# Kernel tuning notes

Hardware: AMD Instinct MI355X
Metric: run time of the kernel (lower is better)

Reference implementation:

```python
import jax, jax.numpy as jnp
import numpy as np

FRAME_T = 8
NUM_K = 10


def _masked_att(att, temp):
    # att: [B, H, P, P] -> softmax over groups of size P//FRAME_T, top-k threshold mask
    B, H, P, _ = att.shape
    D = P // FRAME_T
    a = att.reshape(B, H, P, FRAME_T, D)
    a = jax.nn.softmax(a / temp, axis=-1)
    # k-th largest value per row as threshold (torch.topk values are sorted desc)
    margin = jax.lax.top_k(a, NUM_K)[0][..., -1]  # [B,H,P,FRAME_T]
    a = a * (a >= margin[..., None])
    return a  # [B,H,P,FRAME_T,D]


def setup_inputs() -> dict:
    key = jax.random.key(0)
    k1, k2, k3, k4 = jax.random.split(key, 4)
    B, H, P, hd = 4, 12, 1568, 64
    return {
        "att_s": jax.random.normal(k1, (B, H, P, P), dtype=jnp.float32),
        "att_t": jax.random.normal(k2, (B, H, P, P), dtype=jnp.float32),
        "v_s": jax.random.normal(k3, (B, H, P, hd), dtype=jnp.float32),
        "v_t": jax.random.normal(k4, (B, H, P, hd), dtype=jnp.float32),
    }


def reference(att_s, att_t, v_s, v_t):
    temp = jnp.float32(1.0)
    B, H, P, _ = att_t.shape
    H_s = att_s.shape[1]
    h_dim = v_t.shape[-1]
    D = P // FRAME_T

    a_s = _masked_att(att_s, temp)  # [B,Hs,P,T,D]
    a_t = _masked_att(att_t, temp)  # [B,H,P,T,D]

    vt = v_t.reshape(B, H, D, FRAME_T, h_dim)
    vs = v_s.reshape(B, H_s, D, FRAME_T, h_dim)

    norm_s = a_s.sum(-1)  # [B,Hs,P,T]
    norm_t = a_t.sum(-1)

    o_s = jnp.einsum('bhptd,bhdte->bhpte', a_s, vs) / norm_s[..., None]
    o_t = jnp.einsum('bhptd,bhdte->bhpte', a_t, vt) / norm_t[..., None]

    loss = jnp.mean((o_s - o_t) ** 2)
    return loss
```

## Files before the change

### kernel.cpp

```cpp
#include <hip/hip_runtime.h>
#include <hip/hip_bf16.h>

#define PP 1568
#define TT 8
#define DD 196
#define HD 64
#define NBH 48
#define NROW (NBH*PP*TT)
#define RPW 32
#define WPB 2
#define NWAVE (NROW/RPW)
#define NBLK5 (NWAVE/WPB)
#define NXCD 8
#define CPX (NBLK5/NXCD)
#define NPART NWAVE
#define NRED1 ((NPART+255)/256)
#define SUB (8*DD*4)
#define VSLAB (DD*TT*HD)
#define WPBH 392
#define KMASK 0xFFFFFF00u

typedef float f4 __attribute__((ext_vector_type(4)));
typedef unsigned u4v __attribute__((ext_vector_type(4)));

__device__ __forceinline__ float readlane_f(float v, int l) {
    return __int_as_float(__builtin_amdgcn_readlane(__float_as_int(v), l));
}

__device__ __forceinline__ float wave_sum_u(float v) {
#define STEPS(ctrl) { float t_ = __int_as_float(__builtin_amdgcn_update_dpp( \
        0, __float_as_int(v), ctrl, 0xF, 0xF, true)); v += t_; }
    STEPS(0x111) STEPS(0x112) STEPS(0x114) STEPS(0x118) STEPS(0x142) STEPS(0x143)
#undef STEPS
    return readlane_f(v, 63);
}

__device__ __forceinline__ unsigned UMX(unsigned a, unsigned b){ return a>b?a:b; }
__device__ __forceinline__ unsigned UMN(unsigned a, unsigned b){ return a<b?a:b; }

__device__ __forceinline__ unsigned med3u(unsigned a, unsigned b, unsigned c) {
    unsigned d;
    asm("v_med3_u32 %0, %1, %2, %3" : "=v"(d) : "v"(a), "v"(b), "v"(c));
    return d;
}

__device__ __forceinline__ float untr(unsigned u) {
    return (u & 0x80000000u) ? __uint_as_float(u ^ 0x80000000u)
                             : __uint_as_float(~u);
}

struct K6  { unsigned k0,k1,k2,k3,k4,k5; };
struct K10 { unsigned k0,k1,k2,k3,k4,k5,k6,k7,k8,k9; };
struct MR  { K10 f; unsigned mx; };

#define PUTK6(Q,X,D) { unsigned b_=__float_as_uint(X); \
  unsigned u_=b_^((unsigned)((int)b_>>31)|0x80000000u); \
  unsigned c_=(u_&KMASK)|(unsigned)(D); \
  unsigned n0_=UMX(Q.k0,c_); \
  unsigned n1_=med3u(Q.k0,Q.k1,c_); \
  unsigned n2_=med3u(Q.k1,Q.k2,c_); \
  unsigned n3_=med3u(Q.k2,Q.k3,c_); \
  unsigned n4_=med3u(Q.k3,Q.k4,c_); \
  unsigned n5_=med3u(Q.k4,Q.k5,c_); \
  Q.k0=n0_; Q.k1=n1_; Q.k2=n2_; Q.k3=n3_; Q.k4=n4_; Q.k5=n5_; }
#define PUT4K6(Q,V,D0) PUTK6(Q,(V).x,(D0)) PUTK6(Q,(V).y,(D0)+1) \
                       PUTK6(Q,(V).z,(D0)+2) PUTK6(Q,(V).w,(D0)+3)

__device__ __forceinline__ K6 chain_rows(const char* stg, int a, int b8) {
    K6 q = {0,0,0,0,0,0};
    const char* rb = stg + a*784 + b8*16;
    f4 v;
    v = *(const f4*)(rb);       PUT4K6(q, v, b8*4)
    v = *(const f4*)(rb+128);   PUT4K6(q, v, b8*4+32)
    v = *(const f4*)(rb+256);   PUT4K6(q, v, b8*4+64)
    v = *(const f4*)(rb+384);   PUT4K6(q, v, b8*4+96)
    v = *(const f4*)(rb+512);   PUT4K6(q, v, b8*4+128)
    v = *(const f4*)(rb+640);   PUT4K6(q, v, b8*4+160)
    if (b8 == 7) { v = *(const f4*)(stg + a*784 + 768); PUT4K6(q, v, 192) }
    return q;
}

#define SWZ(x, pat) (unsigned)__builtin_amdgcn_ds_swizzle((int)(x), pat)
__device__ __forceinline__ K6 kshuf8_6(K6 a) {
    K6 r;
    r.k0=SWZ(a.k0,0x201F); r.k1=SWZ(a.k1,0x201F); r.k2=SWZ(a.k2,0x201F);
    r.k3=SWZ(a.k3,0x201F); r.k4=SWZ(a.k4,0x201F); r.k5=SWZ(a.k5,0x201F);
    return r;
}
__device__ __forceinline__ K10 kshuf16(K10 a) {
    K10 r;
    r.k0=SWZ(a.k0,0x401F); r.k1=SWZ(a.k1,0x401F); r.k2=SWZ(a.k2,0x401F);
    r.k3=SWZ(a.k3,0x401F); r.k4=SWZ(a.k4,0x401F); r.k5=SWZ(a.k5,0x401F);
    r.k6=SWZ(a.k6,0x401F); r.k7=SWZ(a.k7,0x401F); r.k8=SWZ(a.k8,0x401F);
    r.k9=SWZ(a.k9,0x401F);
    return r;
}
__device__ __forceinline__ K10 kbp32(K10 a, int bpx) {
    K10 r;
    r.k0=(unsigned)__builtin_amdgcn_ds_bpermute(bpx,(int)a.k0);
    r.k1=(unsigned)__builtin_amdgcn_ds_bpermute(bpx,(int)a.k1);
    r.k2=(unsigned)__builtin_amdgcn_ds_bpermute(bpx,(int)a.k2);
    r.k3=(unsigned)__builtin_amdgcn_ds_bpermute(bpx,(int)a.k3);
    r.k4=(unsigned)__builtin_amdgcn_ds_bpermute(bpx,(int)a.k4);
    r.k5=(unsigned)__builtin_amdgcn_ds_bpermute(bpx,(int)a.k5);
    r.k6=(unsigned)__builtin_amdgcn_ds_bpermute(bpx,(int)a.k6);
    r.k7=(unsigned)__builtin_amdgcn_ds_bpermute(bpx,(int)a.k7);
    r.k8=(unsigned)__builtin_amdgcn_ds_bpermute(bpx,(int)a.k8);
    r.k9=(unsigned)__builtin_amdgcn_ds_bpermute(bpx,(int)a.k9);
    return r;
}

__device__ __forceinline__ K10 kmrg66(K6 A, K6 B) {
    unsigned p00=UMN(A.k0,B.k0);
    unsigned p01=UMN(A.k0,B.k1), p10=UMN(A.k1,B.k0);
    unsigned p02=UMN(A.k0,B.k2), p11=UMN(A.k1,B.k1), p20=UMN(A.k2,B.k0);
    unsigned p03=UMN(A.k0,B.k3), p12=UMN(A.k1,B.k2), p21=UMN(A.k2,B.k1), p30=UMN(A.k3,B.k0);
    unsigned p04=UMN(A.k0,B.k4), p13=UMN(A.k1,B.k3), p22=UMN(A.k2,B.k2), p31=UMN(A.k3,B.k1), p40=UMN(A.k4,B.k0);
    unsigned p05=UMN(A.k0,B.k5), p14=UMN(A.k1,B.k4), p23=UMN(A.k2,B.k3), p32=UMN(A.k3,B.k2), p41=UMN(A.k4,B.k1), p50=UMN(A.k5,B.k0);
    unsigned p15=UMN(A.k1,B.k5), p24=UMN(A.k2,B.k4), p33=UMN(A.k3,B.k3), p42=UMN(A.k4,B.k2), p51=UMN(A.k5,B.k1);
    unsigned p25=UMN(A.k2,B.k5), p34=UMN(A.k3,B.k4), p43=UMN(A.k4,B.k3), p52=UMN(A.k5,B.k2);
    unsigned p35=UMN(A.k3,B.k5), p44=UMN(A.k4,B.k4), p53=UMN(A.k5,B.k3);
    K10 M;
    M.k0=UMX(A.k0,B.k0);
    M.k1=UMX(UMX(A.k1,B.k1),p00);
    M.k2=UMX(UMX(A.k2,B.k2),UMX(p01,p10));
    M.k3=UMX(UMX(A.k3,B.k3),UMX(p02,UMX(p11,p20)));
    M.k4=UMX(UMX(A.k4,B.k4),UMX(UMX(p03,p12),UMX(p21,p30)));
    M.k5=UMX(UMX(A.k5,B.k5),UMX(UMX(p04,p13),UMX(p22,UMX(p31,p40))));
    M.k6=UMX(UMX(p05,p14),UMX(UMX(p23,p32),UMX(p41,p50)));
    M.k7=UMX(UMX(p15,p24),UMX(p33,UMX(p42,p51)));
    M.k8=UMX(UMX(p25,p34),UMX(p43,p52));
    M.k9=UMX(p35,UMX(p44,p53));
    return M;
}

__device__ __forceinline__ K10 kmrg(K10 A, K10 B) {
    unsigned p00=UMN(A.k0,B.k0);
    unsigned p01=UMN(A.k0,B.k1), p10=UMN(A.k1,B.k0);
    unsigned p02=UMN(A.k0,B.k2), p11=UMN(A.k1,B.k1), p20=UMN(A.k2,B.k0);
    unsigned p03=UMN(A.k0,B.k3), p12=UMN(A.k1,B.k2), p21=UMN(A.k2,B.k1), p30=UMN(A.k3,B.k0);
    unsigned p04=UMN(A.k0,B.k4), p13=UMN(A.k1,B.k3), p22=UMN(A.k2,B.k2), p31=UMN(A.k3,B.k1), p40=UMN(A.k4,B.k0);
    unsigned p05=UMN(A.k0,B.k5), p14=UMN(A.k1,B.k4), p23=UMN(A.k2,B.k3), p32=UMN(A.k3,B.k2), p41=UMN(A.k4,B.k1), p50=UMN(A.k5,B.k0);
    unsigned p06=UMN(A.k0,B.k6), p15=UMN(A.k1,B.k5), p24=UMN(A.k2,B.k4), p33=UMN(A.k3,B.k3), p42=UMN(A.k4,B.k2), p51=UMN(A.k5,B.k1), p60=UMN(A.k6,B.k0);
    unsigned p07=UMN(A.k0,B.k7), p16=UMN(A.k1,B.k6), p25=UMN(A.k2,B.k5), p34=UMN(A.k3,B.k4), p43=UMN(A.k4,B.k3), p52=UMN(A.k5,B.k2), p61=UMN(A.k6,B.k1), p70=UMN(A.k7,B.k0);
    unsigned p08=UMN(A.k0,B.k8), p17=UMN(A.k1,B.k7), p26=UMN(A.k2,B.k6), p35=UMN(A.k3,B.k5), p44=UMN(A.k4,B.k4), p53=UMN(A.k5,B.k3), p62=UMN(A.k6,B.k2), p71=UMN(A.k7,B.k1), p80=UMN(A.k8,B.k0);
    K10 M;
    M.k0=UMX(A.k0,B.k0);
    M.k1=UMX(UMX(A.k1,B.k1),p00);
    M.k2=UMX(UMX(A.k2,B.k2),UMX(p01,p10));
    M.k3=UMX(UMX(A.k3,B.k3),UMX(p02,UMX(p11,p20)));
    M.k4=UMX(UMX(A.k4,B.k4),UMX(UMX(p03,p12),UMX(p21,p30)));
    M.k5=UMX(UMX(A.k5,B.k5),UMX(UMX(p04,p13),UMX(p22,UMX(p31,p40))));
    M.k6=UMX(UMX(A.k6,B.k6),UMX(UMX(p05,p14),UMX(UMX(p23,p32),UMX(p41,p50))));
    M.k7=UMX(UMX(A.k7,B.k7),UMX(UMX(UMX(p06,p15),UMX(p24,p33)),UMX(UMX(p42,p51),p60)));
    M.k8=UMX(UMX(A.k8,B.k8),UMX(UMX(UMX(p07,p16),UMX(p25,p34)),UMX(UMX(p43,p52),UMX(p61,p70))));
    M.k9=UMX(UMX(A.k9,B.k9),UMX(UMX(UMX(p08,p17),UMX(p26,p35)),UMX(UMX(p44,p53),UMX(UMX(p62,p71),p80))));
    return M;
}

__device__ __forceinline__ MR merge_all(K6 q, int bpx) {
    K10 m = kmrg66(q, kshuf8_6(q));
    K10 n = kmrg(m, kshuf16(m));
    K10 r = kbp32(n, bpx);
    MR out;
    out.mx = UMX(n.k0, r.k0);
    out.f.k0=UMX(n.k0,r.k9); out.f.k1=UMX(n.k1,r.k8); out.f.k2=UMX(n.k2,r.k7);
    out.f.k3=UMX(n.k3,r.k6); out.f.k4=UMX(n.k4,r.k5); out.f.k5=UMX(n.k5,r.k4);
    out.f.k6=UMX(n.k6,r.k3); out.f.k7=UMX(n.k7,r.k2); out.f.k8=UMX(n.k8,r.k1);
    out.f.k9=UMX(n.k9,r.k0);
    return out;
}

#define LOADR(R, P) { const char* p_=(P); \
    R##0=*(const f4*)(p_+lane*16); \
    R##1=*(const f4*)(p_+1024+lane*16); \
    R##2=*(const f4*)(p_+2048+lane*16); \
    R##3=*(const f4*)(p_+3072+lane*16); \
    R##4=*(const f4*)(p_+4096+lane*16); \
    R##5=*(const f4*)(p_+5120+lane*16); \
    if (lane<8) R##6=*(const f4*)(p_+6144+lane*16); }
#define STORER(R) { \
    *(f4*)(stg+lane*16)=R##0; *(f4*)(stg+1024+lane*16)=R##1; \
    *(f4*)(stg+2048+lane*16)=R##2; *(f4*)(stg+3072+lane*16)=R##3; \
    *(f4*)(stg+4096+lane*16)=R##4; *(f4*)(stg+5120+lane*16)=R##5; \
    if (lane<8) *(f4*)(stg+6144+lane*16)=R##6; }

#define PKW(F,K) ((__float_as_uint(F)&KMASK)|((K)&0xFFu))

__global__ __launch_bounds__(128) void vtop_main(
        const float* __restrict__ att_s, const float* __restrict__ att_t,
        const float* __restrict__ v_s,   const float* __restrict__ v_t,
        float* __restrict__ partial) {
    __shared__ f4  stgv[WPB][SUB/16];
    __shared__ u4v wbuf[WPB][5][RPW];

    int tid  = threadIdx.x;
    int wid  = tid >> 6;
    int lane = tid & 63;
    char* stg = (char*)&stgv[wid][0];
    int a = lane & 7, b8 = lane >> 3;
    int bpx = (lane ^ 32) << 2;

    int blk = (blockIdx.x % NXCD) * CPX + blockIdx.x / NXCD;
    int gwave = blk * WPB + wid;
    int bh = gwave / WPBH;

    const char* baseS = (const char*)att_s + (size_t)gwave * (RPW*DD*4);
    const char* baseT = (const char*)att_t + (size_t)gwave * (RPW*DD*4);

    f4 rs0{},rs1{},rs2{},rs3{},rs4{},rs5{},rs6{};
    f4 rt0{},rt1{},rt2{},rt3{},rt4{},rt5{},rt6{};

    LOADR(rs, baseS)

#pragma unroll 1
    for (int s = 0; s < 4; ++s) {
        STORER(rs)
        LOADR(rt, baseT + s*SUB)
        K6 qS = chain_rows(stg, a, b8);
        MR mS = merge_all(qS, bpx);
        STORER(rt)
        if (s < 3) LOADR(rs, baseS + (s+1)*SUB)
        K6 qT = chain_rows(stg, a, b8);
        MR mT = merge_all(qT, bpx);
        K10 fS = mS.f, fT = mT.f;

        float CS = untr(mS.mx & KMASK), CT = untr(mT.mx & KMASK);
        float wS0=__expf(untr(fS.k0&KMASK)-CS), wS1=__expf(untr(fS.k1&KMASK)-CS),
              wS2=__expf(untr(fS.k2&KMASK)-CS), wS3=__expf(untr(fS.k3&KMASK)-CS),
              wS4=__expf(untr(fS.k4&KMASK)-CS), wS5=__expf(untr(fS.k5&KMASK)-CS),
              wS6=__expf(untr(fS.k6&KMASK)-CS), wS7=__expf(untr(fS.k7&KMASK)-CS),
              wS8=__expf(untr(fS.k8&KMASK)-CS), wS9=__expf(untr(fS.k9&KMASK)-CS);
        float wT0=__expf(untr(fT.k0&KMASK)-CT), wT1=__expf(untr(fT.k1&KMASK)-CT),
              wT2=__expf(untr(fT.k2&KMASK)-CT), wT3=__expf(untr(fT.k3&KMASK)-CT),
              wT4=__expf(untr(fT.k4&KMASK)-CT), wT5=__expf(untr(fT.k5&KMASK)-CT),
              wT6=__expf(untr(fT.k6&KMASK)-CT), wT7=__expf(untr(fT.k7&KMASK)-CT),
              wT8=__expf(untr(fT.k8&KMASK)-CT), wT9=__expf(untr(fT.k9&KMASK)-CT);
        float wsS = (((wS0+wS1)+(wS2+wS3))+((wS4+wS5)+(wS6+wS7)))+(wS8+wS9);
        float wsT = (((wT0+wT1)+(wT2+wT3))+((wT4+wT5)+(wT6+wT7)))+(wT8+wT9);
        float invS =  __builtin_amdgcn_rcpf(wsS);
        float invT = -__builtin_amdgcn_rcpf(wsT);

        if (lane < 8) {
            int row = (s << 3) | lane;
            u4v w;
            w.x=PKW(wS0*invS,fS.k0); w.y=PKW(wS1*invS,fS.k1);
            w.z=PKW(wS2*invS,fS.k2); w.w=PKW(wS3*invS,fS.k3);
            wbuf[wid][0][row]=w;
            w.x=PKW(wS4*invS,fS.k4); w.y=PKW(wS5*invS,fS.k5);
            w.z=PKW(wS6*invS,fS.k6); w.w=PKW(wS7*invS,fS.k7);
            wbuf[wid][1][row]=w;
            w.x=PKW(wS8*invS,fS.k8); w.y=PKW(wS9*invS,fS.k9);
            w.z=PKW(wT0*invT,fT.k0); w.w=PKW(wT1*invT,fT.k1);
            wbuf[wid][2][row]=w;
            w.x=PKW(wT2*invT,fT.k2); w.y=PKW(wT3*invT,fT.k3);
            w.z=PKW(wT4*invT,fT.k4); w.w=PKW(wT5*invT,fT.k5);
            wbuf[wid][3][row]=w;
            w.x=PKW(wT6*invT,fT.k6); w.y=PKW(wT7*invT,fT.k7);
            w.z=PKW(wT8*invT,fT.k8); w.w=PKW(wT9*invT,fT.k9);
            wbuf[wid][4][row]=w;
        }
    }

    const float* vSb = v_s + (size_t)bh * VSLAB;
    const float* vTb = v_t + (size_t)bh * VSLAB;
    float lacc = 0.f;
#pragma unroll 1
    for (int k = 0; k < RPW; ++k) {
        unsigned base = ((unsigned)(k & 7) << 6) + (unsigned)lane;
        u4v w0v=wbuf[wid][0][k], w1v=wbuf[wid][1][k], w2v=wbuf[wid][2][k],
            w3v=wbuf[wid][3][k], w4v=wbuf[wid][4][k];
        float dsum = 0.f;
#define TRM(U, VB) { unsigned u_=(U); \
        float wf_ = __uint_as_float(u_ & KMASK); \
        dsum = fmaf(wf_, VB[((u_ & 0xFFu) << 9) + base], dsum); }
        TRM(w0v.x, vSb) TRM(w0v.y, vSb) TRM(w0v.z, vSb) TRM(w0v.w, vSb)
        TRM(w1v.x, vSb) TRM(w1v.y, vSb) TRM(w1v.z, vSb) TRM(w1v.w, vSb)
        TRM(w2v.x, vSb) TRM(w2v.y, vSb)
        TRM(w2v.z, vTb) TRM(w2v.w, vTb)
        TRM(w3v.x, vTb) TRM(w3v.y, vTb) TRM(w3v.z, vTb) TRM(w3v.w, vTb)
        TRM(w4v.x, vTb) TRM(w4v.y, vTb) TRM(w4v.z, vTb) TRM(w4v.w, vTb)
#undef TRM
        lacc = fmaf(dsum, dsum, lacc);
    }

    float tot = wave_sum_u(lacc);
    if (lane == 0) partial[gwave] = tot;
}

__global__ __launch_bounds__(256) void vtop_reduce1(
        const float* __restrict__ partial, float* __restrict__ p2) {
    int i = blockIdx.x * 256 + threadIdx.x;
    float v = (i < NPART) ? partial[i] : 0.f;
    float wtot = wave_sum_u(v);
    __shared__ float sm[4];
    int lane = threadIdx.x & 63, wid = threadIdx.x >> 6;
    if (lane == 0) sm[wid] = wtot;
    __syncthreads();
    if (threadIdx.x == 0) p2[blockIdx.x] = (sm[0] + sm[1]) + (sm[2] + sm[3]);
}

__global__ __launch_bounds__(256) void vtop_reduce2(
        const float* __restrict__ p2, float* __restrict__ out) {
    __shared__ double smd[256];
    double a = 0.0;
    if (threadIdx.x < NRED1) a = (double)p2[threadIdx.x];
    smd[threadIdx.x] = a;
    __syncthreads();
    for (int s = 128; s > 0; s >>= 1) {
        if (threadIdx.x < s) smd[threadIdx.x] += smd[threadIdx.x + s];
        __syncthreads();
    }
    if (threadIdx.x == 0) {
        const double inv_n = 1.0 / ((double)NBH * PP * TT * HD);
        out[0] = (float)(smd[0] * inv_n);
    }
}

extern "C" void kernel_launch(void* const* d_in, const int* in_sizes, int n_in,
                              void* d_out, int out_size, void* d_ws, size_t ws_size,
                              hipStream_t stream) {
    const float* att_s = (const float*)d_in[0];
    const float* att_t = (const float*)d_in[1];
    const float* v_s   = (const float*)d_in[2];
    const float* v_t   = (const float*)d_in[3];
    float* out     = (float*)d_out;
    float* partial = (float*)d_ws;
    float* p2      = (float*)d_ws + NPART;

    vtop_main<<<NBLK5, 128, 0, stream>>>(att_s, att_t, v_s, v_t, partial);
    vtop_reduce1<<<NRED1, 256, 0, stream>>>(partial, p2);
    vtop_reduce2<<<1, 256, 0, stream>>>(p2, out);
}
```

Baseline: 331.0 us.

## Use float-domain top-k keys and scalarize weight decode in value gather

Top-k keys become floats with the column index packed into the low mantissa bits and are compared with fmaxf/fminf/fmed3f. This drops the sign-flip key transform and its inverse (untr) on the softmax path, and the empty slots now start at a large negative value instead of zero. The value-gather loop reads each packed weight with readfirstlane so the index and weight come from scalar registers, and it splits the dot product across four accumulators to shorten the FMA dependency chain. Float comparison ordering differs slightly from the unsigned order for negative values once low bits are replaced, which could change tie handling.

```diff
diff --git a/kernel.cpp b/kernel.cpp
--- a/kernel.cpp
+++ b/kernel.cpp
@@ -19,6 +19,7 @@
 #define VSLAB (DD*TT*HD)
 #define WPBH 392
 #define KMASK 0xFFFFFF00u
+#define NEG_INF (-3.0e38f)
 
 typedef float f4 __attribute__((ext_vector_type(4)));
 typedef unsigned u4v __attribute__((ext_vector_type(4)));
@@ -35,39 +36,29 @@
     return readlane_f(v, 63);
 }
 
-__device__ __forceinline__ unsigned UMX(unsigned a, unsigned b){ return a>b?a:b; }
-__device__ __forceinline__ unsigned UMN(unsigned a, unsigned b){ return a<b?a:b; }
-
-__device__ __forceinline__ unsigned med3u(unsigned a, unsigned b, unsigned c) {
-    unsigned d;
-    asm("v_med3_u32 %0, %1, %2, %3" : "=v"(d) : "v"(a), "v"(b), "v"(c));
-    return d;
-}
-
-__device__ __forceinline__ float untr(unsigned u) {
-    return (u & 0x80000000u) ? __uint_as_float(u ^ 0x80000000u)
-                             : __uint_as_float(~u);
-}
-
-struct K6  { unsigned k0,k1,k2,k3,k4,k5; };
-struct K10 { unsigned k0,k1,k2,k3,k4,k5,k6,k7,k8,k9; };
-struct MR  { K10 f; unsigned mx; };
-
-#define PUTK6(Q,X,D) { unsigned b_=__float_as_uint(X); \
-  unsigned u_=b_^((unsigned)((int)b_>>31)|0x80000000u); \
-  unsigned c_=(u_&KMASK)|(unsigned)(D); \
-  unsigned n0_=UMX(Q.k0,c_); \
-  unsigned n1_=med3u(Q.k0,Q.k1,c_); \
-  unsigned n2_=med3u(Q.k1,Q.k2,c_); \
-  unsigned n3_=med3u(Q.k2,Q.k3,c_); \
-  unsigned n4_=med3u(Q.k3,Q.k4,c_); \
-  unsigned n5_=med3u(Q.k4,Q.k5,c_); \
+__device__ __forceinline__ float kval(float k) {
+    return __uint_as_float(__float_as_uint(k) & KMASK);
+}
+
+struct K6  { float k0,k1,k2,k3,k4,k5; };
+struct K10 { float k0,k1,k2,k3,k4,k5,k6,k7,k8,k9; };
+struct MR  { K10 f; float mx; };
+
+#define PUTK6(Q,X,D) { \
+  unsigned cu_=(__float_as_uint(X)&KMASK)|(unsigned)(D); \
+  float c_=__uint_as_float(cu_); \
+  float n0_=fmaxf(Q.k0,c_); \
+  float n1_=__builtin_amdgcn_fmed3f(Q.k0,Q.k1,c_); \
+  float n2_=__builtin_amdgcn_fmed3f(Q.k1,Q.k2,c_); \
+  float n3_=__builtin_amdgcn_fmed3f(Q.k2,Q.k3,c_); \
+  float n4_=__builtin_amdgcn_fmed3f(Q.k3,Q.k4,c_); \
+  float n5_=__builtin_amdgcn_fmed3f(Q.k4,Q.k5,c_); \
   Q.k0=n0_; Q.k1=n1_; Q.k2=n2_; Q.k3=n3_; Q.k4=n4_; Q.k5=n5_; }
 #define PUT4K6(Q,V,D0) PUTK6(Q,(V).x,(D0)) PUTK6(Q,(V).y,(D0)+1) \
                        PUTK6(Q,(V).z,(D0)+2) PUTK6(Q,(V).w,(D0)+3)
 
 __device__ __forceinline__ K6 chain_rows(const char* stg, int a, int b8) {
-    K6 q = {0,0,0,0,0,0};
+    K6 q = {NEG_INF,NEG_INF,NEG_INF,NEG_INF,NEG_INF,NEG_INF};
     const char* rb = stg + a*784 + b8*16;
     f4 v;
     v = *(const f4*)(rb);       PUT4K6(q, v, b8*4)
@@ -76,85 +67,82 @@
     v = *(const f4*)(rb+384);   PUT4K6(q, v, b8*4+96)
     v = *(const f4*)(rb+512);   PUT4K6(q, v, b8*4+128)
     v = *(const f4*)(rb+640);   PUT4K6(q, v, b8*4+160)
-    if (b8 == 7) { v = *(const f4*)(stg + a*784 + 768); PUT4K6(q, v, 192) }
+    if (b8 == 7) { f4 w = *(const f4*)(stg + a*784 + 768); PUT4K6(q, w, 192) }
     return q;
 }
 
-#define SWZ(x, pat) (unsigned)__builtin_amdgcn_ds_swizzle((int)(x), pat)
+#define FSWZ(x, pat) __int_as_float(__builtin_amdgcn_ds_swizzle(__float_as_int(x), pat))
 __device__ __forceinline__ K6 kshuf8_6(K6 a) {
     K6 r;
-    r.k0=SWZ(a.k0,0x201F); r.k1=SWZ(a.k1,0x201F); r.k2=SWZ(a.k2,0x201F);
-    r.k3=SWZ(a.k3,0x201F); r.k4=SWZ(a.k4,0x201F); r.k5=SWZ(a.k5,0x201F);
+    r.k0=FSWZ(a.k0,0x201F); r.k1=FSWZ(a.k1,0x201F); r.k2=FSWZ(a.k2,0x201F);
+    r.k3=FSWZ(a.k3,0x201F); r.k4=FSWZ(a.k4,0x201F); r.k5=FSWZ(a.k5,0x201F);
     return r;
 }
 __device__ __forceinline__ K10 kshuf16(K10 a) {
     K10 r;
-    r.k0=SWZ(a.k0,0x401F); r.k1=SWZ(a.k1,0x401F); r.k2=SWZ(a.k2,0x401F);
-    r.k3=SWZ(a.k3,0x401F); r.k4=SWZ(a.k4,0x401F); r.k5=SWZ(a.k5,0x401F);
-    r.k6=SWZ(a.k6,0x401F); r.k7=SWZ(a.k7,0x401F); r.k8=SWZ(a.k8,0x401F);
-    r.k9=SWZ(a.k9,0x401F);
+    r.k0=FSWZ(a.k0,0x401F); r.k1=FSWZ(a.k1,0x401F); r.k2=FSWZ(a.k2,0x401F);
+    r.k3=FSWZ(a.k3,0x401F); r.k4=FSWZ(a.k4,0x401F); r.k5=FSWZ(a.k5,0x401F);
+    r.k6=FSWZ(a.k6,0x401F); r.k7=FSWZ(a.k7,0x401F); r.k8=FSWZ(a.k8,0x401F);
+    r.k9=FSWZ(a.k9,0x401F);
     return r;
+}
+__device__ __forceinline__ float fbp(int bpx, float x) {
+    return __int_as_float(__builtin_amdgcn_ds_bpermute(bpx, __float_as_int(x)));
 }
 __device__ __forceinline__ K10 kbp32(K10 a, int bpx) {
     K10 r;
-    r.k0=(unsigned)__builtin_amdgcn_ds_bpermute(bpx,(int)a.k0);
-    r.k1=(unsigned)__builtin_amdgcn_ds_bpermute(bpx,(int)a.k1);
-    r.k2=(unsigned)__builtin_amdgcn_ds_bpermute(bpx,(int)a.k2);
-    r.k3=(unsigned)__builtin_amdgcn_ds_bpermute(bpx,(int)a.k3);
-    r.k4=(unsigned)__builtin_amdgcn_ds_bpermute(bpx,(int)a.k4);
-    r.k5=(unsigned)__builtin_amdgcn_ds_bpermute(bpx,(int)a.k5);
-    r.k6=(unsigned)__builtin_amdgcn_ds_bpermute(bpx,(int)a.k6);
-    r.k7=(unsigned)__builtin_amdgcn_ds_bpermute(bpx,(int)a.k7);
-    r.k8=(unsigned)__builtin_amdgcn_ds_bpermute(bpx,(int)a.k8);
-    r.k9=(unsigned)__builtin_amdgcn_ds_bpermute(bpx,(int)a.k9);
+    r.k0=fbp(bpx,a.k0); r.k1=fbp(bpx,a.k1); r.k2=fbp(bpx,a.k2);
+    r.k3=fbp(bpx,a.k3); r.k4=fbp(bpx,a.k4); r.k5=fbp(bpx,a.k5);
+    r.k6=fbp(bpx,a.k6); r.k7=fbp(bpx,a.k7); r.k8=fbp(bpx,a.k8);
+    r.k9=fbp(bpx,a.k9);
     return r;
 }
 
 __device__ __forceinline__ K10 kmrg66(K6 A, K6 B) {
-    unsigned p00=UMN(A.k0,B.k0);
-    unsigned p01=UMN(A.k0,B.k1), p10=UMN(A.k1,B.k0);
-    unsigned p02=UMN(A.k0,B.k2), p11=UMN(A.k1,B.k1), p20=UMN(A.k2,B.k0);
-    unsigned p03=UMN(A.k0,B.k3), p12=UMN(A.k1,B.k2), p21=UMN(A.k2,B.k1), p30=UMN(A.k3,B.k0);
-    unsigned p04=UMN(A.k0,B.k4), p13=UMN(A.k1,B.k3), p22=UMN(A.k2,B.k2), p31=UMN(A.k3,B.k1), p40=UMN(A.k4,B.k0);
-    unsigned p05=UMN(A.k0,B.k5), p14=UMN(A.k1,B.k4), p23=UMN(A.k2,B.k3), p32=UMN(A.k3,B.k2), p41=UMN(A.k4,B.k1), p50=UMN(A.k5,B.k0);
-    unsigned p15=UMN(A.k1,B.k5), p24=UMN(A.k2,B.k4), p33=UMN(A.k3,B.k3), p42=UMN(A.k4,B.k2), p51=UMN(A.k5,B.k1);
-    unsigned p25=UMN(A.k2,B.k5), p34=UMN(A.k3,B.k4), p43=UMN(A.k4,B.k3), p52=UMN(A.k5,B.k2);
-    unsigned p35=UMN(A.k3,B.k5), p44=UMN(A.k4,B.k4), p53=UMN(A.k5,B.k3);
+    float p00=fminf(A.k0,B.k0);
+    float p01=fminf(A.k0,B.k1), p10=fminf(A.k1,B.k0);
+    float p02=fminf(A.k0,B.k2), p11=fminf(A.k1,B.k1), p20=fminf(A.k2,B.k0);
+    float p03=fminf(A.k0,B.k3), p12=fminf(A.k1,B.k2), p21=fminf(A.k2,B.k1), p30=fminf(A.k3,B.k0);
+    float p04=fminf(A.k0,B.k4), p13=fminf(A.k1,B.k3), p22=fminf(A.k2,B.k2), p31=fminf(A.k3,B.k1), p40=fminf(A.k4,B.k0);
+    float p05=fminf(A.k0,B.k5), p14=fminf(A.k1,B.k4), p23=fminf(A.k2,B.k3), p32=fminf(A.k3,B.k2), p41=fminf(A.k4,B.k1), p50=fminf(A.k5,B.k0);
+    float p15=fminf(A.k1,B.k5), p24=fminf(A.k2,B.k4), p33=fminf(A.k3,B.k3), p42=fminf(A.k4,B.k2), p51=fminf(A.k5,B.k1);
+    float p25=fminf(A.k2,B.k5), p34=fminf(A.k3,B.k4), p43=fminf(A.k4,B.k3), p52=fminf(A.k5,B.k2);
+    float p35=fminf(A.k3,B.k5), p44=fminf(A.k4,B.k4), p53=fminf(A.k5,B.k3);
     K10 M;
-    M.k0=UMX(A.k0,B.k0);
-    M.k1=UMX(UMX(A.k1,B.k1),p00);
-    M.k2=UMX(UMX(A.k2,B.k2),UMX(p01,p10));
-    M.k3=UMX(UMX(A.k3,B.k3),UMX(p02,UMX(p11,p20)));
-    M.k4=UMX(UMX(A.k4,B.k4),UMX(UMX(p03,p12),UMX(p21,p30)));
-    M.k5=UMX(UMX(A.k5,B.k5),UMX(UMX(p04,p13),UMX(p22,UMX(p31,p40))));
-    M.k6=UMX(UMX(p05,p14),UMX(UMX(p23,p32),UMX(p41,p50)));
-    M.k7=UMX(UMX(p15,p24),UMX(p33,UMX(p42,p51)));
-    M.k8=UMX(UMX(p25,p34),UMX(p43,p52));
-    M.k9=UMX(p35,UMX(p44,p53));
+    M.k0=fmaxf(A.k0,B.k0);
+    M.k1=fmaxf(fmaxf(A.k1,B.k1),p00);
+    M.k2=fmaxf(fmaxf(A.k2,B.k2),fmaxf(p01,p10));
+    M.k3=fmaxf(fmaxf(A.k3,B.k3),fmaxf(p02,fmaxf(p11,p20)));
+    M.k4=fmaxf(fmaxf(A.k4,B.k4),fmaxf(fmaxf(p03,p12),fmaxf(p21,p30)));
+    M.k5=fmaxf(fmaxf(A.k5,B.k5),fmaxf(fmaxf(p04,p13),fmaxf(p22,fmaxf(p31,p40))));
+    M.k6=fmaxf(fmaxf(p05,p14),fmaxf(fmaxf(p23,p32),fmaxf(p41,p50)));
+    M.k7=fmaxf(fmaxf(p15,p24),fmaxf(p33,fmaxf(p42,p51)));
+    M.k8=fmaxf(fmaxf(p25,p34),fmaxf(p43,p52));
+    M.k9=fmaxf(p35,fmaxf(p44,p53));
     return M;
 }
 
 __device__ __forceinline__ K10 kmrg(K10 A, K10 B) {
-    unsigned p00=UMN(A.k0,B.k0);
-    unsigned p01=UMN(A.k0,B.k1), p10=UMN(A.k1,B.k0);
-    unsigned p02=UMN(A.k0,B.k2), p11=UMN(A.k1,B.k1), p20=UMN(A.k2,B.k0);
-    unsigned p03=UMN(A.k0,B.k3), p12=UMN(A.k1,B.k2), p21=UMN(A.k2,B.k1), p30=UMN(A.k3,B.k0);
-    unsigned p04=UMN(A.k0,B.k4), p13=UMN(A.k1,B.k3), p22=UMN(A.k2,B.k2), p31=UMN(A.k3,B.k1), p40=UMN(A.k4,B.k0);
-    unsigned p05=UMN(A.k0,B.k5), p14=UMN(A.k1,B.k4), p23=UMN(A.k2,B.k3), p32=UMN(A.k3,B.k2), p41=UMN(A.k4,B.k1), p50=UMN(A.k5,B.k0);
-    unsigned p06=UMN(A.k0,B.k6), p15=UMN(A.k1,B.k5), p24=UMN(A.k2,B.k4), p33=UMN(A.k3,B.k3), p42=UMN(A.k4,B.k2), p51=UMN(A.k5,B.k1), p60=UMN(A.k6,B.k0);
-    unsigned p07=UMN(A.k0,B.k7), p16=UMN(A.k1,B.k6), p25=UMN(A.k2,B.k5), p34=UMN(A.k3,B.k4), p43=UMN(A.k4,B.k3), p52=UMN(A.k5,B.k2), p61=UMN(A.k6,B.k1), p70=UMN(A.k7,B.k0);
-    unsigned p08=UMN(A.k0,B.k8), p17=UMN(A.k1,B.k7), p26=UMN(A.k2,B.k6), p35=UMN(A.k3,B.k5), p44=UMN(A.k4,B.k4), p53=UMN(A.k5,B.k3), p62=UMN(A.k6,B.k2), p71=UMN(A.k7,B.k1), p80=UMN(A.k8,B.k0);
+    float p00=fminf(A.k0,B.k0);
+    float p01=fminf(A.k0,B.k1), p10=fminf(A.k1,B.k0);
+    float p02=fminf(A.k0,B.k2), p11=fminf(A.k1,B.k1), p20=fminf(A.k2,B.k0);
+    float p03=fminf(A.k0,B.k3), p12=fminf(A.k1,B.k2), p21=fminf(A.k2,B.k1), p30=fminf(A.k3,B.k0);
+    float p04=fminf(A.k0,B.k4), p13=fminf(A.k1,B.k3), p22=fminf(A.k2,B.k2), p31=fminf(A.k3,B.k1), p40=fminf(A.k4,B.k0);
+    float p05=fminf(A.k0,B.k5), p14=fminf(A.k1,B.k4), p23=fminf(A.k2,B.k3), p32=fminf(A.k3,B.k2), p41=fminf(A.k4,B.k1), p50=fminf(A.k5,B.k0);
+    float p06=fminf(A.k0,B.k6), p15=fminf(A.k1,B.k5), p24=fminf(A.k2,B.k4), p33=fminf(A.k3,B.k3), p42=fminf(A.k4,B.k2), p51=fminf(A.k5,B.k1), p60=fminf(A.k6,B.k0);
+    float p07=fminf(A.k0,B.k7), p16=fminf(A.k1,B.k6), p25=fminf(A.k2,B.k5), p34=fminf(A.k3,B.k4), p43=fminf(A.k4,B.k3), p52=fminf(A.k5,B.k2), p61=fminf(A.k6,B.k1), p70=fminf(A.k7,B.k0);
+    float p08=fminf(A.k0,B.k8), p17=fminf(A.k1,B.k7), p26=fminf(A.k2,B.k6), p35=fminf(A.k3,B.k5), p44=fminf(A.k4,B.k4), p53=fminf(A.k5,B.k3), p62=fminf(A.k6,B.k2), p71=fminf(A.k7,B.k1), p80=fminf(A.k8,B.k0);
     K10 M;
-    M.k0=UMX(A.k0,B.k0);
-    M.k1=UMX(UMX(A.k1,B.k1),p00);
-    M.k2=UMX(UMX(A.k2,B.k2),UMX(p01,p10));
-    M.k3=UMX(UMX(A.k3,B.k3),UMX(p02,UMX(p11,p20)));
-    M.k4=UMX(UMX(A.k4,B.k4),UMX(UMX(p03,p12),UMX(p21,p30)));
-    M.k5=UMX(UMX(A.k5,B.k5),UMX(UMX(p04,p13),UMX(p22,UMX(p31,p40))));
-    M.k6=UMX(UMX(A.k6,B.k6),UMX(UMX(p05,p14),UMX(UMX(p23,p32),UMX(p41,p50))));
-    M.k7=UMX(UMX(A.k7,B.k7),UMX(UMX(UMX(p06,p15),UMX(p24,p33)),UMX(UMX(p42,p51),p60)));
-    M.k8=UMX(UMX(A.k8,B.k8),UMX(UMX(UMX(p07,p16),UMX(p25,p34)),UMX(UMX(p43,p52),UMX(p61,p70))));
-    M.k9=UMX(UMX(A.k9,B.k9),UMX(UMX(UMX(p08,p17),UMX(p26,p35)),UMX(UMX(p44,p53),UMX(UMX(p62,p71),p80))));
+    M.k0=fmaxf(A.k0,B.k0);
+    M.k1=fmaxf(fmaxf(A.k1,B.k1),p00);
+    M.k2=fmaxf(fmaxf(A.k2,B.k2),fmaxf(p01,p10));
+    M.k3=fmaxf(fmaxf(A.k3,B.k3),fmaxf(p02,fmaxf(p11,p20)));
+    M.k4=fmaxf(fmaxf(A.k4,B.k4),fmaxf(fmaxf(p03,p12),fmaxf(p21,p30)));
+    M.k5=fmaxf(fmaxf(A.k5,B.k5),fmaxf(fmaxf(p04,p13),fmaxf(p22,fmaxf(p31,p40))));
+    M.k6=fmaxf(fmaxf(A.k6,B.k6),fmaxf(fmaxf(p05,p14),fmaxf(fmaxf(p23,p32),fmaxf(p41,p50))));
+    M.k7=fmaxf(fmaxf(A.k7,B.k7),fmaxf(fmaxf(fmaxf(p06,p15),fmaxf(p24,p33)),fmaxf(fmaxf(p42,p51),p60)));
+    M.k8=fmaxf(fmaxf(A.k8,B.k8),fmaxf(fmaxf(fmaxf(p07,p16),fmaxf(p25,p34)),fmaxf(fmaxf(p43,p52),fmaxf(p61,p70))));
+    M.k9=fmaxf(fmaxf(A.k9,B.k9),fmaxf(fmaxf(fmaxf(p08,p17),fmaxf(p26,p35)),fmaxf(fmaxf(p44,p53),fmaxf(fmaxf(p62,p71),p80))));
     return M;
 }
 
@@ -163,11 +151,11 @@
     K10 n = kmrg(m, kshuf16(m));
     K10 r = kbp32(n, bpx);
     MR out;
-    out.mx = UMX(n.k0, r.k0);
-    out.f.k0=UMX(n.k0,r.k9); out.f.k1=UMX(n.k1,r.k8); out.f.k2=UMX(n.k2,r.k7);
-    out.f.k3=UMX(n.k3,r.k6); out.f.k4=UMX(n.k4,r.k5); out.f.k5=UMX(n.k5,r.k4);
-    out.f.k6=UMX(n.k6,r.k3); out.f.k7=UMX(n.k7,r.k2); out.f.k8=UMX(n.k8,r.k1);
-    out.f.k9=UMX(n.k9,r.k0);
+    out.mx = fmaxf(n.k0, r.k0);
+    out.f.k0=fmaxf(n.k0,r.k9); out.f.k1=fmaxf(n.k1,r.k8); out.f.k2=fmaxf(n.k2,r.k7);
+    out.f.k3=fmaxf(n.k3,r.k6); out.f.k4=fmaxf(n.k4,r.k5); out.f.k5=fmaxf(n.k5,r.k4);
+    out.f.k6=fmaxf(n.k6,r.k3); out.f.k7=fmaxf(n.k7,r.k2); out.f.k8=fmaxf(n.k8,r.k1);
+    out.f.k9=fmaxf(n.k9,r.k0);
     return out;
 }
 
@@ -185,7 +173,7 @@
     *(f4*)(stg+4096+lane*16)=R##4; *(f4*)(stg+5120+lane*16)=R##5; \
     if (lane<8) *(f4*)(stg+6144+lane*16)=R##6; }
 
-#define PKW(F,K) ((__float_as_uint(F)&KMASK)|((K)&0xFFu))
+#define PKW(F,K) ((__float_as_uint(F)&KMASK)|(__float_as_uint(K)&0xFFu))
 
 __global__ __launch_bounds__(128) void vtop_main(
         const float* __restrict__ att_s, const float* __restrict__ att_t,
@@ -225,17 +213,17 @@
         MR mT = merge_all(qT, bpx);
         K10 fS = mS.f, fT = mT.f;
 
-        float CS = untr(mS.mx & KMASK), CT = untr(mT.mx & KMASK);
-        float wS0=__expf(untr(fS.k0&KMASK)-CS), wS1=__expf(untr(fS.k1&KMASK)-CS),
-              wS2=__expf(untr(fS.k2&KMASK)-CS), wS3=__expf(untr(fS.k3&KMASK)-CS),
-              wS4=__expf(untr(fS.k4&KMASK)-CS), wS5=__expf(untr(fS.k5&KMASK)-CS),
-              wS6=__expf(untr(fS.k6&KMASK)-CS), wS7=__expf(untr(fS.k7&KMASK)-CS),
-              wS8=__expf(untr(fS.k8&KMASK)-CS), wS9=__expf(untr(fS.k9&KMASK)-CS);
-        float wT0=__expf(untr(fT.k0&KMASK)-CT), wT1=__expf(untr(fT.k1&KMASK)-CT),
-              wT2=__expf(untr(fT.k2&KMASK)-CT), wT3=__expf(untr(fT.k3&KMASK)-CT),
-              wT4=__expf(untr(fT.k4&KMASK)-CT), wT5=__expf(untr(fT.k5&KMASK)-CT),
-              wT6=__expf(untr(fT.k6&KMASK)-CT), wT7=__expf(untr(fT.k7&KMASK)-CT),
-              wT8=__expf(untr(fT.k8&KMASK)-CT), wT9=__expf(untr(fT.k9&KMASK)-CT);
+        float CS = kval(mS.mx), CT = kval(mT.mx);
+        float wS0=__expf(kval(fS.k0)-CS), wS1=__expf(kval(fS.k1)-CS),
+              wS2=__expf(kval(fS.k2)-CS), wS3=__expf(kval(fS.k3)-CS),
+              wS4=__expf(kval(fS.k4)-CS), wS5=__expf(kval(fS.k5)-CS),
+              wS6=__expf(kval(fS.k6)-CS), wS7=__expf(kval(fS.k7)-CS),
+              wS8=__expf(kval(fS.k8)-CS), wS9=__expf(kval(fS.k9)-CS);
+        float wT0=__expf(kval(fT.k0)-CT), wT1=__expf(kval(fT.k1)-CT),
+              wT2=__expf(kval(fT.k2)-CT), wT3=__expf(kval(fT.k3)-CT),
+              wT4=__expf(kval(fT.k4)-CT), wT5=__expf(kval(fT.k5)-CT),
+              wT6=__expf(kval(fT.k6)-CT), wT7=__expf(kval(fT.k7)-CT),
+              wT8=__expf(kval(fT.k8)-CT), wT9=__expf(kval(fT.k9)-CT);
         float wsS = (((wS0+wS1)+(wS2+wS3))+((wS4+wS5)+(wS6+wS7)))+(wS8+wS9);
         float wsT = (((wT0+wT1)+(wT2+wT3))+((wT4+wT5)+(wT6+wT7)))+(wT8+wT9);
         float invS =  __builtin_amdgcn_rcpf(wsS);
@@ -264,23 +252,27 @@
 
     const float* vSb = v_s + (size_t)bh * VSLAB;
     const float* vTb = v_t + (size_t)bh * VSLAB;
+    unsigned ul = (unsigned)lane;
     float lacc = 0.f;
 #pragma unroll 1
     for (int k = 0; k < RPW; ++k) {
-        unsigned base = ((unsigned)(k & 7) << 6) + (unsigned)lane;
+        unsigned t64 = ((unsigned)(k & 7) << 6);
+        const float* vSk = vSb + t64;
+        const float* vTk = vTb + t64;
         u4v w0v=wbuf[wid][0][k], w1v=wbuf[wid][1][k], w2v=wbuf[wid][2][k],
             w3v=wbuf[wid][3][k], w4v=wbuf[wid][4][k];
-        float dsum = 0.f;
-#define TRM(U, VB) { unsigned u_=(U); \
-        float wf_ = __uint_as_float(u_ & KMASK); \
-        dsum = fmaf(wf_, VB[((u_ & 0xFFu) << 9) + base], dsum); }
-        TRM(w0v.x, vSb) TRM(w0v.y, vSb) TRM(w0v.z, vSb) TRM(w0v.w, vSb)
-        TRM(w1v.x, vSb) TRM(w1v.y, vSb) TRM(w1v.z, vSb) TRM(w1v.w, vSb)
-        TRM(w2v.x, vSb) TRM(w2v.y, vSb)
-        TRM(w2v.z, vTb) TRM(w2v.w, vTb)
-        TRM(w3v.x, vTb) TRM(w3v.y, vTb) TRM(w3v.z, vTb) TRM(w3v.w, vTb)
-        TRM(w4v.x, vTb) TRM(w4v.y, vTb) TRM(w4v.z, vTb) TRM(w4v.w, vTb)
+        float d0=0.f, d1=0.f, d2=0.f, d3=0.f;
+#define TRM(U, VB, ACC) { unsigned pk_=(unsigned)__builtin_amdgcn_readfirstlane((int)(U)); \
+        float wf_ = __uint_as_float(pk_ & KMASK); \
+        ACC = fmaf(wf_, VB[((pk_ & 0xFFu) << 9) + ul], ACC); }
+        TRM(w0v.x, vSk, d0) TRM(w0v.y, vSk, d1) TRM(w0v.z, vSk, d2) TRM(w0v.w, vSk, d3)
+        TRM(w1v.x, vSk, d0) TRM(w1v.y, vSk, d1) TRM(w1v.z, vSk, d2) TRM(w1v.w, vSk, d3)
+        TRM(w2v.x, vSk, d0) TRM(w2v.y, vSk, d1)
+        TRM(w2v.z, vTk, d2) TRM(w2v.w, vTk, d3)
+        TRM(w3v.x, vTk, d0) TRM(w3v.y, vTk, d1) TRM(w3v.z, vTk, d2) TRM(w3v.w, vTk, d3)
+        TRM(w4v.x, vTk, d0) TRM(w4v.y, vTk, d1) TRM(w4v.z, vTk, d2) TRM(w4v.w, vTk, d3)
 #undef TRM
+        float dsum = (d0 + d1) + (d2 + d3);
         lacc = fmaf(dsum, dsum, lacc);
     }
 
```

Measured after the change: 323.7 us. 1.02x faster.
